# Kernel optimization log

Measured on AMD Instinct MI355X. Metric: run time of the kernel, lower is better.

Reference implementation:

```python
import jax, jax.numpy as jnp
import numpy as np

B, H = 2048, 1024
P_DROP = 0.6


def setup_inputs() -> dict:
    key = jax.random.key(0)
    ks = jax.random.split(key, 17)
    stdv = 1.0 / np.sqrt(H)
    u = lambda k, shape: jax.random.uniform(k, shape, jnp.float32, -stdv, stdv)
    inp = {
        'input': jax.random.normal(ks[0], (B, H), jnp.float32),
        'hidden': jax.random.normal(ks[1], (B, H), jnp.float32),
        'pre_cell': jax.random.normal(ks[2], (B, H), jnp.float32),
        # weights are (hidden_size, input_size) and used as input @ W (requires H == input_size)
        'w_i': u(ks[3], (H, H)), 'w_f': u(ks[4], (H, H)),
        'w_o': u(ks[5], (H, H)), 'w_c': u(ks[6], (H, H)),
        'u_i': u(ks[7], (H, H)), 'u_f': u(ks[8], (H, H)),
        'u_o': u(ks[9], (H, H)), 'u_c': u(ks[10], (H, H)),
        'bias1': u(ks[11], (H,)), 'bias2': u(ks[12], (H,)),
        'bias3': u(ks[13], (H,)), 'bias4': u(ks[14], (H,)),
    }
    # F.dropout(training=True) mask, pre-scaled by 1/(1-p); shape matches h_t [B,1,H]
    keep = jax.random.bernoulli(ks[15], 1.0 - P_DROP, (B, 1, H))
    inp['drop_mask'] = keep.astype(jnp.float32) / (1.0 - P_DROP)
    return inp


def reference(input, hidden, pre_cell, w_i, w_f, w_o, w_c, u_i, u_f, u_o, u_c,
              bias1, bias2, bias3, bias4, drop_mask):
    # Fuse the 8 small GEMMs into 2 big ones: gate order (f, i, o, c)
    Wx = jnp.concatenate([w_f, w_i, w_o, w_c], axis=1)   # [H, 4H]
    Wh = jnp.concatenate([u_f, u_i, u_o, u_c], axis=1)   # [H, 4H]
    b = jnp.concatenate([bias1, bias2, bias3, bias4])    # [4H]
    gates = input @ Wx + hidden @ Wh + b                 # [B, 4H]
    f_t, i_t, o_t, g_t = jnp.split(gates, 4, axis=1)
    f_t = jax.nn.sigmoid(f_t)
    i_t = jax.nn.sigmoid(i_t)
    o_t = jax.nn.sigmoid(o_t)
    g_t = jnp.tanh(g_t)
    c_t = pre_cell * f_t + i_t * g_t                     # [B, H]
    h_t = o_t * jnp.tanh(c_t)                            # [B, H]
    h_t = h_t[:, None, :] * drop_mask                    # dropout (training=True)
    c_t = c_t[:, None, :]
    return h_t, c_t
```

## Files before the change

### kernel.cpp

```cpp
#include <hip/hip_runtime.h>
#include <hip/hip_bf16.h>
#include <cstdint>

#define B_DIM 2048
#define H_DIM 1024
#define K_DIM 2048
#define N_DIM 4096

typedef unsigned short u16;
typedef __attribute__((ext_vector_type(8))) short bf16x8;
typedef __attribute__((ext_vector_type(4))) float f32x4;

__device__ __forceinline__ u16 f2bf(float f) {
    unsigned int u = __float_as_uint(f);
    u += 0x7FFFu + ((u >> 16) & 1u);
    return (u16)(u >> 16);
}

__device__ __forceinline__ float sigmoid_f(float x) {
    return 1.0f / (1.0f + __expf(-x));
}

__global__ __launch_bounds__(256) void pack_A(const float* __restrict__ input,
                                              const float* __restrict__ hidden,
                                              u16* __restrict__ A) {
    int idx = (blockIdx.x * 256 + threadIdx.x) * 4;
    int m = idx >> 11;
    int k = idx & (K_DIM - 1);
    const float* src = (k < H_DIM) ? (input + (size_t)m * H_DIM + k)
                                   : (hidden + (size_t)m * H_DIM + (k - H_DIM));
    float4 v = *(const float4*)src;
    ushort4 o;
    o.x = f2bf(v.x); o.y = f2bf(v.y); o.z = f2bf(v.z); o.w = f2bf(v.w);
    *(ushort4*)(A + idx) = o;
}

__global__ __launch_bounds__(256) void pack_B(
    const float* __restrict__ w_f, const float* __restrict__ w_i,
    const float* __restrict__ w_o, const float* __restrict__ w_c,
    const float* __restrict__ u_f, const float* __restrict__ u_i,
    const float* __restrict__ u_o, const float* __restrict__ u_c,
    u16* __restrict__ Bt) {
    __shared__ float tile[32][33];
    const int z = blockIdx.z;
    const float* M;
    switch (z) {
        case 0: M = w_f; break;
        case 1: M = w_i; break;
        case 2: M = w_o; break;
        case 3: M = w_c; break;
        case 4: M = u_f; break;
        case 5: M = u_i; break;
        case 6: M = u_o; break;
        default: M = u_c; break;
    }
    const int g = z & 3;
    const int half = z >> 2;
    const int h0 = blockIdx.x * 32;
    const int k0 = blockIdx.y * 32;
    const int tx = threadIdx.x;
    const int ty = threadIdx.y;
#pragma unroll
    for (int r = 0; r < 4; r++)
        tile[ty + r * 8][tx] = M[(size_t)(k0 + ty + r * 8) * H_DIM + h0 + tx];
    __syncthreads();
#pragma unroll
    for (int r = 0; r < 4; r++) {
        int n = g * H_DIM + h0 + ty + r * 8;
        Bt[(size_t)n * K_DIM + half * H_DIM + k0 + tx] = f2bf(tile[tx][ty + r * 8]);
    }
}

#define BM 128
#define BN 128
#define BK 32
#define LDSW 40

__global__ __launch_bounds__(256, 2) void gemm_bt(const u16* __restrict__ A,
                                                  const u16* __restrict__ Bt,
                                                  float* __restrict__ C) {
    __shared__ u16 As[BM * LDSW];
    __shared__ u16 Bs[BN * LDSW];
    const int t = threadIdx.x;
    const int m0 = blockIdx.y * BM;
    const int n0 = blockIdx.x * BN;
    const int wave = t >> 6;
    const int lane = t & 63;
    const int wr = wave >> 1;
    const int wc = wave & 1;
    const int lrow = lane & 15;
    const int quad = lane >> 4;

    f32x4 acc[4][4] = {};

    const int r0 = t >> 2;
    const int c0 = (t & 3) * 8;
    const u16* Ag0 = A + (size_t)(m0 + r0) * K_DIM + c0;
    const u16* Ag1 = Ag0 + (size_t)64 * K_DIM;
    const u16* Bg0 = Bt + (size_t)(n0 + r0) * K_DIM + c0;
    const u16* Bg1 = Bg0 + (size_t)64 * K_DIM;
    u16* As0 = As + r0 * LDSW + c0;
    u16* As1 = As0 + 64 * LDSW;
    u16* Bs0 = Bs + r0 * LDSW + c0;
    u16* Bs1 = Bs0 + 64 * LDSW;

    const u16* afr = As + (wr * 64 + lrow) * LDSW + quad * 8;
    const u16* bfr = Bs + (wc * 64 + lrow) * LDSW + quad * 8;

    for (int k0 = 0; k0 < K_DIM; k0 += BK) {
        int4 a0 = *(const int4*)(Ag0 + k0);
        int4 a1 = *(const int4*)(Ag1 + k0);
        int4 b0 = *(const int4*)(Bg0 + k0);
        int4 b1 = *(const int4*)(Bg1 + k0);
        __syncthreads();
        *(int4*)As0 = a0;
        *(int4*)As1 = a1;
        *(int4*)Bs0 = b0;
        *(int4*)Bs1 = b1;
        __syncthreads();
        bf16x8 af[4], bf[4];
#pragma unroll
        for (int i = 0; i < 4; i++) af[i] = *(const bf16x8*)(afr + i * 16 * LDSW);
#pragma unroll
        for (int j = 0; j < 4; j++) bf[j] = *(const bf16x8*)(bfr + j * 16 * LDSW);
#pragma unroll
        for (int i = 0; i < 4; i++)
#pragma unroll
            for (int j = 0; j < 4; j++)
                acc[i][j] = __builtin_amdgcn_mfma_f32_16x16x32_bf16(
                    af[i], bf[j], acc[i][j], 0, 0, 0);
    }

    const int crow = m0 + wr * 64 + quad * 4;
    const int ccol = n0 + wc * 64 + lrow;
#pragma unroll
    for (int i = 0; i < 4; i++)
#pragma unroll
        for (int j = 0; j < 4; j++) {
#pragma unroll
            for (int r = 0; r < 4; r++)
                C[(size_t)(crow + i * 16 + r) * N_DIM + ccol + j * 16] = acc[i][j][r];
        }
}

__global__ __launch_bounds__(256) void lstm_epilogue(
    const float* __restrict__ gates, const float* __restrict__ pre_cell,
    const float* __restrict__ b1, const float* __restrict__ b2,
    const float* __restrict__ b3, const float* __restrict__ b4,
    const float* __restrict__ mask, float* __restrict__ out) {
    int idx = (blockIdx.x * 256 + threadIdx.x) * 4;
    int m = idx >> 10;
    int h = idx & (H_DIM - 1);
    const float* grow = gates + (size_t)m * N_DIM + h;
    float4 gf = *(const float4*)(grow);
    float4 gi = *(const float4*)(grow + H_DIM);
    float4 go = *(const float4*)(grow + 2 * H_DIM);
    float4 gg = *(const float4*)(grow + 3 * H_DIM);
    float4 vb1 = *(const float4*)(b1 + h);
    float4 vb2 = *(const float4*)(b2 + h);
    float4 vb3 = *(const float4*)(b3 + h);
    float4 vb4 = *(const float4*)(b4 + h);
    float4 pc = *(const float4*)(pre_cell + idx);
    float4 mk = *(const float4*)(mask + idx);

    float4 oh, oc;
    const float* pgf = (const float*)&gf;
    const float* pgi = (const float*)&gi;
    const float* pgo = (const float*)&go;
    const float* pgg = (const float*)&gg;
    const float* pb1 = (const float*)&vb1;
    const float* pb2 = (const float*)&vb2;
    const float* pb3 = (const float*)&vb3;
    const float* pb4 = (const float*)&vb4;
    const float* ppc = (const float*)&pc;
    const float* pmk = (const float*)&mk;
    float* poh = (float*)&oh;
    float* poc = (float*)&oc;
#pragma unroll
    for (int q = 0; q < 4; q++) {
        float fv = sigmoid_f(pgf[q] + pb1[q]);
        float iv = sigmoid_f(pgi[q] + pb2[q]);
        float ov = sigmoid_f(pgo[q] + pb3[q]);
        float gv = tanhf(pgg[q] + pb4[q]);
        float cv = ppc[q] * fv + iv * gv;
        poc[q] = cv;
        poh[q] = ov * tanhf(cv) * pmk[q];
    }
    *(float4*)(out + idx) = oh;
    *(float4*)(out + (size_t)B_DIM * H_DIM + idx) = oc;
}

extern "C" void kernel_launch(void* const* d_in, const int* in_sizes, int n_in,
                              void* d_out, int out_size, void* d_ws, size_t ws_size,
                              hipStream_t stream) {
    const float* input    = (const float*)d_in[0];
    const float* hidden   = (const float*)d_in[1];
    const float* pre_cell = (const float*)d_in[2];
    const float* w_i = (const float*)d_in[3];
    const float* w_f = (const float*)d_in[4];
    const float* w_o = (const float*)d_in[5];
    const float* w_c = (const float*)d_in[6];
    const float* u_i = (const float*)d_in[7];
    const float* u_f = (const float*)d_in[8];
    const float* u_o = (const float*)d_in[9];
    const float* u_c = (const float*)d_in[10];
    const float* b1  = (const float*)d_in[11];
    const float* b2  = (const float*)d_in[12];
    const float* b3  = (const float*)d_in[13];
    const float* b4  = (const float*)d_in[14];
    const float* mask = (const float*)d_in[15];
    float* out = (float*)d_out;

    char* ws = (char*)d_ws;
    u16*  A     = (u16*)ws;
    u16*  Bt    = (u16*)(ws + (size_t)8 * 1024 * 1024);
    float* gates = (float*)(ws + (size_t)24 * 1024 * 1024);

    pack_A<<<dim3((B_DIM * K_DIM) / (256 * 4)), dim3(256), 0, stream>>>(input, hidden, A);
    pack_B<<<dim3(32, 32, 8), dim3(32, 8), 0, stream>>>(w_f, w_i, w_o, w_c,
                                                        u_f, u_i, u_o, u_c, Bt);
    gemm_bt<<<dim3(N_DIM / BN, B_DIM / BM), dim3(256), 0, stream>>>(A, Bt, gates);
    lstm_epilogue<<<dim3((B_DIM * H_DIM) / (256 * 4)), dim3(256), 0, stream>>>(
        gates, pre_cell, b1, b2, b3, b4, mask, out);
}
```

Measured before the change: 189.9 us.

## Fuse LSTM epilogue into GEMM with gate-interleaved weights and async LDS loads

Interleaves the four gate columns in the packed weight matrix so each GEMM tile holds all four gates for its hidden units. The epilogue then runs inside the GEMM, bias is folded into the accumulator init, and the fp32 gates buffer round trip is gone. Global-to-LDS loads now use direct global_load_lds without padding, which may cause LDS bank conflicts. Also vectorizes pack_B and swaps in exp-based tanh.

```diff
diff --git a/kernel.cpp b/kernel.cpp
--- a/kernel.cpp
+++ b/kernel.cpp
@@ -9,6 +9,7 @@
 
 typedef unsigned short u16;
 typedef __attribute__((ext_vector_type(8))) short bf16x8;
+typedef __attribute__((ext_vector_type(8))) unsigned short u16x8;
 typedef __attribute__((ext_vector_type(4))) float f32x4;
 
 __device__ __forceinline__ u16 f2bf(float f) {
@@ -19,6 +20,18 @@
 
 __device__ __forceinline__ float sigmoid_f(float x) {
     return 1.0f / (1.0f + __expf(-x));
+}
+
+__device__ __forceinline__ float tanh_f(float x) {
+    float e = __expf(2.0f * x);
+    return 1.0f - 2.0f / (e + 1.0f);
+}
+
+__device__ __forceinline__ void async16(const u16* g, u16* l) {
+    __builtin_amdgcn_global_load_lds(
+        (const __attribute__((address_space(1))) unsigned int*)g,
+        (__attribute__((address_space(3))) unsigned int*)l,
+        16, 0, 0);
 }
 
 __global__ __launch_bounds__(256) void pack_A(const float* __restrict__ input,
@@ -41,7 +54,7 @@
     const float* __restrict__ u_f, const float* __restrict__ u_i,
     const float* __restrict__ u_o, const float* __restrict__ u_c,
     u16* __restrict__ Bt) {
-    __shared__ float tile[32][33];
+    __shared__ float tile[32][65];
     const int z = blockIdx.z;
     const float* M;
     switch (z) {
@@ -57,72 +70,96 @@
     const int g = z & 3;
     const int half = z >> 2;
     const int h0 = blockIdx.x * 32;
-    const int k0 = blockIdx.y * 32;
-    const int tx = threadIdx.x;
-    const int ty = threadIdx.y;
-#pragma unroll
-    for (int r = 0; r < 4; r++)
-        tile[ty + r * 8][tx] = M[(size_t)(k0 + ty + r * 8) * H_DIM + h0 + tx];
+    const int k0 = blockIdx.y * 64;
+    const int t = threadIdx.x;
+#pragma unroll
+    for (int it = 0; it < 2; it++) {
+        int kl = (t >> 3) + it * 32;
+        int hl = (t & 7) * 4;
+        float4 v = *(const float4*)(M + (size_t)(k0 + kl) * H_DIM + h0 + hl);
+        tile[hl + 0][kl] = v.x;
+        tile[hl + 1][kl] = v.y;
+        tile[hl + 2][kl] = v.z;
+        tile[hl + 3][kl] = v.w;
+    }
     __syncthreads();
-#pragma unroll
-    for (int r = 0; r < 4; r++) {
-        int n = g * H_DIM + h0 + ty + r * 8;
-        Bt[(size_t)n * K_DIM + half * H_DIM + k0 + tx] = f2bf(tile[tx][ty + r * 8]);
-    }
+    {
+        int hl = t >> 3;
+        int ko = (t & 7) * 8;
+        u16x8 o;
+#pragma unroll
+        for (int q = 0; q < 8; q++) o[q] = f2bf(tile[hl][ko + q]);
+        size_t n = 4 * (size_t)(h0 + hl) + g;
+        *(u16x8*)(Bt + n * K_DIM + half * H_DIM + k0 + ko) = o;
+    }
+}
+
+__global__ __launch_bounds__(256) void pack_bias(
+    const float* __restrict__ b1, const float* __restrict__ b2,
+    const float* __restrict__ b3, const float* __restrict__ b4,
+    float* __restrict__ bias_il) {
+    int idx = blockIdx.x * 256 + threadIdx.x;
+    int h = idx >> 2, g = idx & 3;
+    const float* b = (g == 0) ? b1 : (g == 1) ? b2 : (g == 2) ? b3 : b4;
+    bias_il[idx] = b[h];
 }
 
 #define BM 128
 #define BN 128
 #define BK 32
-#define LDSW 40
-
-__global__ __launch_bounds__(256, 2) void gemm_bt(const u16* __restrict__ A,
-                                                  const u16* __restrict__ Bt,
-                                                  float* __restrict__ C) {
-    __shared__ u16 As[BM * LDSW];
-    __shared__ u16 Bs[BN * LDSW];
+
+__global__ __launch_bounds__(256, 2) void gemm_fused(
+    const u16* __restrict__ A, const u16* __restrict__ Bt,
+    const float* __restrict__ bias_il, const float* __restrict__ pre_cell,
+    const float* __restrict__ mask, float* __restrict__ out) {
+    __shared__ char smem[17408];
+    u16* As = (u16*)smem;
+    u16* Bs = (u16*)(smem + 8192);
+    float* et = (float*)smem;
+
     const int t = threadIdx.x;
+    const int w = t >> 6, l = t & 63;
     const int m0 = blockIdx.y * BM;
     const int n0 = blockIdx.x * BN;
-    const int wave = t >> 6;
-    const int lane = t & 63;
-    const int wr = wave >> 1;
-    const int wc = wave & 1;
-    const int lrow = lane & 15;
-    const int quad = lane >> 4;
-
-    f32x4 acc[4][4] = {};
-
-    const int r0 = t >> 2;
-    const int c0 = (t & 3) * 8;
-    const u16* Ag0 = A + (size_t)(m0 + r0) * K_DIM + c0;
+    const int wr = w >> 1;
+    const int wc = w & 1;
+    const int lrow = l & 15;
+    const int quad = l >> 4;
+
+    const int sr = w * 16 + (l >> 2);
+    const int sc = (l & 3) * 8;
+    const u16* Ag0 = A + (size_t)(m0 + sr) * K_DIM + sc;
     const u16* Ag1 = Ag0 + (size_t)64 * K_DIM;
-    const u16* Bg0 = Bt + (size_t)(n0 + r0) * K_DIM + c0;
+    const u16* Bg0 = Bt + (size_t)(n0 + sr) * K_DIM + sc;
     const u16* Bg1 = Bg0 + (size_t)64 * K_DIM;
-    u16* As0 = As + r0 * LDSW + c0;
-    u16* As1 = As0 + 64 * LDSW;
-    u16* Bs0 = Bs + r0 * LDSW + c0;
-    u16* Bs1 = Bs0 + 64 * LDSW;
-
-    const u16* afr = As + (wr * 64 + lrow) * LDSW + quad * 8;
-    const u16* bfr = Bs + (wc * 64 + lrow) * LDSW + quad * 8;
+    u16* Al0 = As + sr * BK + sc;
+    u16* Al1 = Al0 + 64 * BK;
+    u16* Bl0 = Bs + sr * BK + sc;
+    u16* Bl1 = Bl0 + 64 * BK;
+
+    const u16* afr = As + (wr * 64 + lrow) * BK + quad * 8;
+    const u16* bfr = Bs + (wc * 64 + lrow) * BK + quad * 8;
+
+    f32x4 acc[4][4];
+#pragma unroll
+    for (int j = 0; j < 4; j++) {
+        float bv = bias_il[n0 + wc * 64 + j * 16 + lrow];
+#pragma unroll
+        for (int i = 0; i < 4; i++) acc[i][j] = (f32x4){bv, bv, bv, bv};
+    }
 
     for (int k0 = 0; k0 < K_DIM; k0 += BK) {
-        int4 a0 = *(const int4*)(Ag0 + k0);
-        int4 a1 = *(const int4*)(Ag1 + k0);
-        int4 b0 = *(const int4*)(Bg0 + k0);
-        int4 b1 = *(const int4*)(Bg1 + k0);
-        __syncthreads();
-        *(int4*)As0 = a0;
-        *(int4*)As1 = a1;
-        *(int4*)Bs0 = b0;
-        *(int4*)Bs1 = b1;
+        __syncthreads();
+        async16(Ag0 + k0, Al0);
+        async16(Ag1 + k0, Al1);
+        async16(Bg0 + k0, Bl0);
+        async16(Bg1 + k0, Bl1);
         __syncthreads();
         bf16x8 af[4], bf[4];
 #pragma unroll
-        for (int i = 0; i < 4; i++) af[i] = *(const bf16x8*)(afr + i * 16 * LDSW);
-#pragma unroll
-        for (int j = 0; j < 4; j++) bf[j] = *(const bf16x8*)(bfr + j * 16 * LDSW);
+        for (int i = 0; i < 4; i++) af[i] = *(const bf16x8*)(afr + i * 16 * BK);
+#pragma unroll
+        for (int j = 0; j < 4; j++) bf[j] = *(const bf16x8*)(bfr + j * 16 * BK);
 #pragma unroll
         for (int i = 0; i < 4; i++)
 #pragma unroll
@@ -131,63 +168,41 @@
                     af[i], bf[j], acc[i][j], 0, 0, 0);
     }
 
-    const int crow = m0 + wr * 64 + quad * 4;
-    const int ccol = n0 + wc * 64 + lrow;
-#pragma unroll
-    for (int i = 0; i < 4; i++)
-#pragma unroll
-        for (int j = 0; j < 4; j++) {
+    const int row = t >> 1;
+    const int half = t & 1;
+    const size_t orow = (size_t)(m0 + row) * H_DIM;
+#pragma unroll
+    for (int j = 0; j < 4; j++) {
+        __syncthreads();
+#pragma unroll
+        for (int i = 0; i < 4; i++)
 #pragma unroll
             for (int r = 0; r < 4; r++)
-                C[(size_t)(crow + i * 16 + r) * N_DIM + ccol + j * 16] = acc[i][j][r];
+                et[(wr * 64 + i * 16 + quad * 4 + r) * 33 + wc * 16 + lrow] =
+                    acc[i][j][r];
+        __syncthreads();
+        const int hg0 = (n0 >> 2) + half * 16 + j * 4;
+        const float* ep = et + row * 33 + half * 16;
+        float4 pc = *(const float4*)(pre_cell + orow + hg0);
+        float4 mk = *(const float4*)(mask + orow + hg0);
+        const float* ppc = (const float*)&pc;
+        const float* pmk = (const float*)&mk;
+        float4 oh, oc;
+        float* poh = (float*)&oh;
+        float* poc = (float*)&oc;
+#pragma unroll
+        for (int q = 0; q < 4; q++) {
+            float fv = sigmoid_f(ep[4 * q + 0]);
+            float iv = sigmoid_f(ep[4 * q + 1]);
+            float ov = sigmoid_f(ep[4 * q + 2]);
+            float gv = tanh_f(ep[4 * q + 3]);
+            float cv = ppc[q] * fv + iv * gv;
+            poc[q] = cv;
+            poh[q] = ov * tanh_f(cv) * pmk[q];
         }
-}
-
-__global__ __launch_bounds__(256) void lstm_epilogue(
-    const float* __restrict__ gates, const float* __restrict__ pre_cell,
-    const float* __restrict__ b1, const float* __restrict__ b2,
-    const float* __restrict__ b3, const float* __restrict__ b4,
-    const float* __restrict__ mask, float* __restrict__ out) {
-    int idx = (blockIdx.x * 256 + threadIdx.x) * 4;
-    int m = idx >> 10;
-    int h = idx & (H_DIM - 1);
-    const float* grow = gates + (size_t)m * N_DIM + h;
-    float4 gf = *(const float4*)(grow);
-    float4 gi = *(const float4*)(grow + H_DIM);
-    float4 go = *(const float4*)(grow + 2 * H_DIM);
-    float4 gg = *(const float4*)(grow + 3 * H_DIM);
-    float4 vb1 = *(const float4*)(b1 + h);
-    float4 vb2 = *(const float4*)(b2 + h);
-    float4 vb3 = *(const float4*)(b3 + h);
-    float4 vb4 = *(const float4*)(b4 + h);
-    float4 pc = *(const float4*)(pre_cell + idx);
-    float4 mk = *(const float4*)(mask + idx);
-
-    float4 oh, oc;
-    const float* pgf = (const float*)&gf;
-    const float* pgi = (const float*)&gi;
-    const float* pgo = (const float*)&go;
-    const float* pgg = (const float*)&gg;
-    const float* pb1 = (const float*)&vb1;
-    const float* pb2 = (const float*)&vb2;
-    const float* pb3 = (const float*)&vb3;
-    const float* pb4 = (const float*)&vb4;
-    const float* ppc = (const float*)&pc;
-    const float* pmk = (const float*)&mk;
-    float* poh = (float*)&oh;
-    float* poc = (float*)&oc;
-#pragma unroll
-    for (int q = 0; q < 4; q++) {
-        float fv = sigmoid_f(pgf[q] + pb1[q]);
-        float iv = sigmoid_f(pgi[q] + pb2[q]);
-        float ov = sigmoid_f(pgo[q] + pb3[q]);
-        float gv = tanhf(pgg[q] + pb4[q]);
-        float cv = ppc[q] * fv + iv * gv;
-        poc[q] = cv;
-        poh[q] = ov * tanhf(cv) * pmk[q];
-    }
-    *(float4*)(out + idx) = oh;
-    *(float4*)(out + (size_t)B_DIM * H_DIM + idx) = oc;
+        *(float4*)(out + orow + hg0) = oh;
+        *(float4*)(out + (size_t)B_DIM * H_DIM + orow + hg0) = oc;
+    }
 }
 
 extern "C" void kernel_launch(void* const* d_in, const int* in_sizes, int n_in,
@@ -212,14 +227,14 @@
     float* out = (float*)d_out;
 
     char* ws = (char*)d_ws;
-    u16*  A     = (u16*)ws;
-    u16*  Bt    = (u16*)(ws + (size_t)8 * 1024 * 1024);
-    float* gates = (float*)(ws + (size_t)24 * 1024 * 1024);
+    u16*   A       = (u16*)ws;
+    u16*   Bt      = (u16*)(ws + (size_t)8 * 1024 * 1024);
+    float* bias_il = (float*)(ws + (size_t)24 * 1024 * 1024);
 
     pack_A<<<dim3((B_DIM * K_DIM) / (256 * 4)), dim3(256), 0, stream>>>(input, hidden, A);
-    pack_B<<<dim3(32, 32, 8), dim3(32, 8), 0, stream>>>(w_f, w_i, w_o, w_c,
-                                                        u_f, u_i, u_o, u_c, Bt);
-    gemm_bt<<<dim3(N_DIM / BN, B_DIM / BM), dim3(256), 0, stream>>>(A, Bt, gates);
-    lstm_epilogue<<<dim3((B_DIM * H_DIM) / (256 * 4)), dim3(256), 0, stream>>>(
-        gates, pre_cell, b1, b2, b3, b4, mask, out);
-}
+    pack_B<<<dim3(32, 16, 8), dim3(256), 0, stream>>>(w_f, w_i, w_o, w_c,
+                                                      u_f, u_i, u_o, u_c, Bt);
+    pack_bias<<<dim3(16), dim3(256), 0, stream>>>(b1, b2, b3, b4, bias_il);
+    gemm_fused<<<dim3(N_DIM / BN, B_DIM / BM), dim3(256), 0, stream>>>(
+        A, Bt, bias_il, pre_cell, mask, out);
+}
```

New measurement: 179.5 us. 5.4% less time.
